# Performance work log

Hardware: AMD Instinct MI355X
Metric: run time of the kernel (lower is better)

The kernel has to match this reference:

```python
import jax, jax.numpy as jnp
import numpy as np

T, B, IN, OUT = 128, 32, 128, 128
N, M, R, H = 256, 64, 4, 256  # mem_slot, mem_size, read_heads, nn_output_size


def setup_inputs() -> dict:
    key = jax.random.key(0)
    ks = jax.random.split(key, 10)
    s = 0.05
    return {
        "xs": jax.random.normal(ks[0], (T, B, IN), jnp.float32),
        "mem0": jax.random.normal(ks[1], (B, N, M), jnp.float32) * s,
        "W_lstm": jax.random.normal(ks[2], (IN + M * R + H, 4 * H), jnp.float32) * s,
        "b_lstm": jnp.zeros((4 * H,), jnp.float32),
        "W_pre": jax.random.normal(ks[3], (H, OUT), jnp.float32) * s,
        "b_pre": jnp.zeros((OUT,), jnp.float32),
        "W_key": jax.random.normal(ks[4], (H, M), jnp.float32) * s,
        "W_beta": jax.random.normal(ks[5], (H, 1), jnp.float32) * s,
        "W_teach": jax.random.normal(ks[6], (H, M), jnp.float32) * s,
        "W_ro": jax.random.normal(ks[7], (M * R, OUT), jnp.float32) * s,
    }


def reference(xs, mem0, W_lstm, b_lstm, W_pre, b_pre, W_key, W_beta, W_teach, W_ro):
    eps = 1e-8

    def step(carry, x):
        mem, h, c, read_vecs, loss = carry
        # controller: LSTM cell over [x, flattened read vectors]
        inp = jnp.concatenate([x, read_vecs.reshape(B, M * R)], axis=-1)
        z = jnp.concatenate([inp, h], axis=-1) @ W_lstm + b_lstm
        i, f, g, o = jnp.split(z, 4, axis=-1)
        c = jax.nn.sigmoid(f) * c + jax.nn.sigmoid(i) * jnp.tanh(g)
        h = jax.nn.sigmoid(o) * jnp.tanh(c)
        pre_out = h @ W_pre + b_pre          # (B, OUT)
        k = h @ W_key                        # (B, M) content key
        beta = jax.nn.softplus(h @ W_beta)   # (B, 1) sharpness
        teacher = h @ W_teach                # (B, M) generated teacher vec
        # cosine similarity between each memory slot and the key
        num = jnp.einsum('bnm,bm->bn', mem, k)
        den = jnp.maximum(
            jnp.linalg.norm(mem, axis=-1) * jnp.linalg.norm(k, axis=-1, keepdims=True), eps)
        sim = num / den                      # (B, N)
        write_w = jax.nn.softmax(beta * sim, axis=-1)  # safe_softmax over slots
        # additive content write (outer product of write weights and key)
        mem = mem + write_w[:, :, None] * k[:, None, :]
        # supervision loss: match generated teacher to written content
        loss = loss + jnp.mean((k - teacher) ** 2)
        # read: write_w broadcast over R heads -> identical reads per head
        read = jnp.einsum('bn,bnm->bm', write_w, mem)  # (B, M)
        read_vecs = jnp.broadcast_to(read[:, :, None], (B, M, R))
        out = pre_out + read_vecs.reshape(B, M * R) @ W_ro
        return (mem, h, c, read_vecs, loss), out

    carry0 = (mem0,
              jnp.zeros((B, H), xs.dtype),
              jnp.zeros((B, H), xs.dtype),
              jnp.zeros((B, M, R), xs.dtype),
              jnp.zeros((), xs.dtype))
    (_, _, _, _, sup_loss), ys = jax.lax.scan(step, carry0, xs)
    return ys, sup_loss
```

## Files before the change

kernel.cpp:

```cpp
#include <hip/hip_runtime.h>

typedef unsigned short u16;
typedef unsigned long long u64;
typedef short short8 __attribute__((ext_vector_type(8)));
typedef float f32x4 __attribute__((ext_vector_type(4)));

__device__ __forceinline__ float b2f(u16 u) {
    unsigned x = ((unsigned)u) << 16;
    return __builtin_bit_cast(float, x);
}
__device__ __forceinline__ u16 f2b(float f) {
    unsigned u = __builtin_bit_cast(unsigned, f);
    u += 0x7FFFu + ((u >> 16) & 1u);
    return (u16)(u >> 16);
}
__device__ __forceinline__ float sigm(float x) { return 1.f / (1.f + __expf(-x)); }
__device__ __forceinline__ float tanh_(float x) { return 1.f - 2.f / (__expf(2.f * x) + 1.f); }

__device__ __forceinline__ uint4 ldg_cv(const void* p) {
    uint4 v;
    asm volatile("global_load_dwordx4 %0, %1, off sc0 sc1\n\ts_waitcnt vmcnt(0)"
                 : "=v"(v) : "v"(p) : "memory");
    return v;
}
__device__ __forceinline__ void ldg_cv4_issue(const void* p0, const void* p1, const void* p2,
                                              const void* p3, uint4& a, uint4& b, uint4& c, uint4& d) {
    asm volatile(
        "global_load_dwordx4 %0, %4, off sc0 sc1\n\t"
        "global_load_dwordx4 %1, %5, off sc0 sc1\n\t"
        "global_load_dwordx4 %2, %6, off sc0 sc1\n\t"
        "global_load_dwordx4 %3, %7, off sc0 sc1"
        : "=v"(a), "=v"(b), "=v"(c), "=v"(d)
        : "v"(p0), "v"(p1), "v"(p2), "v"(p3) : "memory");
}
__device__ __forceinline__ void wait_vm0() {
    asm volatile("s_waitcnt vmcnt(0)" ::: "memory");
}
__device__ __forceinline__ void stg_cv(void* p, uint4 v) {
    u64 lo = ((u64)v.y << 32) | (u64)v.x;
    u64 hi = ((u64)v.w << 32) | (u64)v.z;
    __hip_atomic_store((u64*)p,     lo, __ATOMIC_RELAXED, __HIP_MEMORY_SCOPE_AGENT);
    __hip_atomic_store((u64*)p + 1, hi, __ATOMIC_RELAXED, __HIP_MEMORY_SCOPE_AGENT);
}

#define T_STEPS 128
#define BATCH   32
#define KHR     320
#define PADK    328
#define MEMPAD  68
#define WKPAD   264

#define WS_BAR      0
#define WS_LOSS     128
#define WS_FLAG     160
#define WS_HRG      192
#define WS_ZSET     41088
#define WS_XSF      41216
#define WS_MEM0F    2138368
#define WS_WLF      4235520
#define WS_BLF      6856960
#define WS_WPREF    6861056
#define WS_BPREF    6992128
#define WS_WKEYF    6992640
#define WS_WBETAF   7058176
#define WS_WTEACHF  7059200
#define WS_WROF     7124736
#define WS_XW       7255808
#define WS_WREFF    24033024
#define WS_WKT      24295168
#define WS_WROEFF   24360704
#define WS_HS       24393472
#define WS_RS       28587776

#define HR_OFF   0
#define WF_OFF   20992
#define WK_OFF   41472
#define MEM_OFF  75264
#define Z_OFF    144896
#define C_OFF    149504
#define KV_OFF   151552
#define WW_OFF   151808
#define KP_OFF   152832
#define RP_OFF   153856
#define BR_OFF   154880
#define WR_OFF   154944
#define SC_OFF   155008
#define WB_OFF   155072
#define HST_OFF  156096
#define RST_OFF  156608
#define LDS_TOTAL 156736

__device__ __forceinline__ void gridbar(unsigned* flags, unsigned phase) {
    __syncthreads();
    if (threadIdx.x < 64) {
        if (threadIdx.x == 0)
            __hip_atomic_store(flags + blockIdx.x, phase, __ATOMIC_RELAXED,
                               __HIP_MEMORY_SCOPE_AGENT);
        long guard = 0;
        for (;;) {
            unsigned v = __hip_atomic_load(flags + (threadIdx.x & 31), __ATOMIC_RELAXED,
                                           __HIP_MEMORY_SCOPE_AGENT);
            if (__ballot(v < phase) == 0ull) break;
            if (++guard > 2000000L) break;
            __builtin_amdgcn_s_sleep(1);
        }
    }
    __syncthreads();
}

__global__ void dnc_probe(const u16* __restrict__ xs_u16, char* __restrict__ ws) {
    __shared__ int cnt;
    if (threadIdx.x == 0) cnt = 0;
    __syncthreads();
    int c = 0;
    for (int i = threadIdx.x; i < 1024; i += 256) {
        int e = (xs_u16[i] >> 7) & 0xFF;
        if (e >= 96 && e <= 135) c++;
    }
    atomicAdd(&cnt, c);
    __syncthreads();
    if (threadIdx.x == 0) *(int*)(ws + WS_FLAG) = (cnt > 820) ? 1 : 0;
}

__global__ void dnc_normalize(const void* s0, const void* s1, const void* s2, const void* s3,
                              const void* s4, const void* s5, const void* s6, const void* s7,
                              const void* s8, const void* s9, char* __restrict__ ws) {
    const void* srcs[10] = {s0, s1, s2, s3, s4, s5, s6, s7, s8, s9};
    const int sizes[10] = {524288, 524288, 655360, 1024, 32768, 128, 16384, 256, 16384, 32768};
    const int bases[10] = {WS_XSF, WS_MEM0F, WS_WLF, WS_BLF, WS_WPREF, WS_BPREF,
                           WS_WKEYF, WS_WBETAF, WS_WTEACHF, WS_WROF};
    const int bf = *(const int*)(ws + WS_FLAG);
    const int gt = blockIdx.x * 256 + threadIdx.x, gs = gridDim.x * 256;
    for (int s = 0; s < 10; ++s) {
        float* dst = (float*)(ws + bases[s]);
        const int n = sizes[s];
        if (bf) {
            const u16* p = (const u16*)srcs[s];
            for (int i = gt; i < n; i += gs) dst[i] = b2f(p[i]);
        } else {
            const float* p = (const float*)srcs[s];
            for (int i = gt; i < n; i += gs) dst[i] = p[i];
        }
    }
}

__global__ void dnc_prologue(char* __restrict__ ws) {
    extern __shared__ float xls[];
    const float* XSF     = (const float*)(ws + WS_XSF);
    const float* WLF     = (const float*)(ws + WS_WLF);
    const float* BLF     = (const float*)(ws + WS_BLF);
    const float* WKEYF   = (const float*)(ws + WS_WKEYF);
    const float* WTEACHF = (const float*)(ws + WS_WTEACHF);
    const float* WROF    = (const float*)(ws + WS_WROF);
    float* xW  = (float*)(ws + WS_XW);
    float* WrE = (float*)(ws + WS_WREFF);
    float* Wkt = (float*)(ws + WS_WKT);
    float* Wre = (float*)(ws + WS_WROEFF);
    const int wg = blockIdx.x, tid = threadIdx.x;
    if (wg < 256) {
        const int rb = wg >> 3, cb = wg & 7;
        const float4* xsrc = (const float4*)(XSF + (size_t)rb * 16384);
        for (int i = tid; i < 4096; i += 256) {
            float4 v = xsrc[i];
            int row = i >> 5, c4 = (i & 31) * 4;
            float* d = xls + row * 129 + c4;
            d[0] = v.x; d[1] = v.y; d[2] = v.z; d[3] = v.w;
        }
        __syncthreads();
        const int tr = tid >> 4, tc = tid & 15;
        const int c0 = cb * 128 + tc * 8;
        float acc[8][8];
#pragma unroll
        for (int rr = 0; rr < 8; ++rr)
#pragma unroll
            for (int cc = 0; cc < 8; ++cc) acc[rr][cc] = BLF[c0 + cc];
        for (int k = 0; k < 128; ++k) {
            float4 wA = *(const float4*)(WLF + (size_t)k * 1024 + c0);
            float4 wB = *(const float4*)(WLF + (size_t)k * 1024 + c0 + 4);
            float w[8] = {wA.x, wA.y, wA.z, wA.w, wB.x, wB.y, wB.z, wB.w};
#pragma unroll
            for (int rr = 0; rr < 8; ++rr) {
                float xv = xls[(tr * 8 + rr) * 129 + k];
#pragma unroll
                for (int cc = 0; cc < 8; ++cc) acc[rr][cc] += xv * w[cc];
            }
        }
#pragma unroll
        for (int rr = 0; rr < 8; ++rr) {
            size_t o = (size_t)(rb * 128 + tr * 8 + rr) * 1024 + c0;
            *(float4*)(xW + o)     = make_float4(acc[rr][0], acc[rr][1], acc[rr][2], acc[rr][3]);
            *(float4*)(xW + o + 4) = make_float4(acc[rr][4], acc[rr][5], acc[rr][6], acc[rr][7]);
        }
    } else if (wg < 320) {
        const int m = wg - 256;
        const int c = tid * 4;
#pragma unroll
        for (int e = 0; e < 4; ++e) {
            float s = 0.f;
#pragma unroll
            for (int rr = 0; rr < 4; ++rr) s += WLF[(size_t)(128 + 4 * m + rr) * 1024 + c + e];
            WrE[m * 1024 + c + e] = s;
        }
    } else if (wg < 336) {
        const int i = (wg - 320) * 1024 + tid * 4;
#pragma unroll
        for (int e = 0; e < 4; ++e) Wkt[i + e] = WKEYF[i + e] - WTEACHF[i + e];
    } else if (wg < 344) {
        const int i = (wg - 336) * 1024 + tid * 4;
#pragma unroll
        for (int e = 0; e < 4; ++e) {
            int m = (i + e) >> 7, c = (i + e) & 127;
            float s = 0.f;
#pragma unroll
            for (int rr = 0; rr < 4; ++rr) s += WROF[(4 * m + rr) * 128 + c];
            Wre[i + e] = s;
        }
    }
}

__global__ __launch_bounds__(256, 1) void dnc_main(char* __restrict__ ws) {
    extern __shared__ char smem[];
    u16*   hr_lds = (u16*)(smem + HR_OFF);
    u16*   wfrag  = (u16*)(smem + WF_OFF);
    u16*   wkeyT  = (u16*)(smem + WK_OFF);
    float* memA   = (float*)(smem + MEM_OFF);
    float* z_lds  = (float*)(smem + Z_OFF);
    float* c_lds  = (float*)(smem + C_OFF);
    float* kv     = (float*)(smem + KV_OFF);
    float* wwts   = (float*)(smem + WW_OFF);
    float* kpart  = (float*)(smem + KP_OFF);
    float* rp     = (float*)(smem + RP_OFF);
    float* bred   = (float*)(smem + BR_OFF);
    float* wred   = (float*)(smem + WR_OFF);
    float* sc     = (float*)(smem + SC_OFF);
    float* wbF    = (float*)(smem + WB_OFF);
    u16*   hstage = (u16*)(smem + HST_OFF);
    u16*   rstage = (u16*)(smem + RST_OFF);

    const int tid  = threadIdx.x;
    const int wg   = blockIdx.x;
    const int lane = tid & 63;
    const int wid  = tid >> 6;

    unsigned* flags = (unsigned*)(ws + WS_BAR);
    u16* hrg        = (u16*)(ws + WS_HRG);
    const float* xWF     = (const float*)(ws + WS_XW);
    const float* WrEffF  = (const float*)(ws + WS_WREFF);
    const float* WLF     = (const float*)(ws + WS_WLF);
    const float* WKEYF   = (const float*)(ws + WS_WKEYF);
    const float* WBETAF  = (const float*)(ws + WS_WBETAF);
    const float* MEM0F   = (const float*)(ws + WS_MEM0F);
    float* HsF = (float*)(ws + WS_HS);
    float* RsF = (float*)(ws + WS_RS);

    for (int i = tid; i < 32 * PADK; i += 256) hr_lds[i] = 0;
    for (int idx = tid; idx < 10240; idx += 256) {
        int k = idx >> 5, c = idx & 31;
        int kt = k >> 5, q = (k >> 3) & 3, j = k & 7;
        int gcol = (c >> 3) * 256 + wg * 8 + (c & 7);
        float v = (k < 64) ? WrEffF[k * 1024 + gcol]
                           : WLF[(size_t)(384 + (k - 64)) * 1024 + gcol];
        wfrag[((kt * 4 + q) * 32 + c) * 8 + j] = f2b(v);
    }
    for (int i = tid; i < 256 * 64; i += 256) {
        int k = i >> 6, m = i & 63;
        wkeyT[m * WKPAD + k] = f2b(WKEYF[i]);
    }
    wbF[tid]   = WBETAF[tid];
    c_lds[tid] = 0.f;
    for (int i = tid; i < 256 * 64; i += 256) {
        int n = i >> 6, m = i & 63;
        memA[n * MEMPAD + m] = MEM0F[wg * 16384 + i];
    }
    __syncthreads();

    const int bt = wid & 1, ct = wid >> 1;
    const int fm = lane & 15, fq = lane >> 4;
    const int pb = tid >> 3, pu = tid & 7;
    unsigned bar_phase = 0;

    float xg0, xg1, xg2, xg3;
    {
        const size_t xb = (size_t)pb * 1024 + wg * 8 + pu;
        xg0 = xWF[xb]; xg1 = xWF[xb + 256]; xg2 = xWF[xb + 512]; xg3 = xWF[xb + 768];
    }
    f32x4 hWacc = {0.f, 0.f, 0.f, 0.f};

    for (int t = 0; t < T_STEPS; ++t) {
        {
            uint4 rv = ldg_cv(hrg + pb * KHR + pu * 8);
            *(uint4*)(hr_lds + pb * PADK + pu * 8) = rv;
        }
        __syncthreads();

        f32x4 acc = hWacc;
#pragma unroll
        for (int kt = 0; kt < 2; ++kt) {
            short8 a = *(const short8*)(hr_lds + (bt * 16 + fm) * PADK + kt * 32 + fq * 8);
            short8 b = *(const short8*)(wfrag + ((kt * 4 + fq) * 32 + ct * 16 + fm) * 8);
            acc = __builtin_amdgcn_mfma_f32_16x16x32_bf16(a, b, acc, 0, 0, 0);
        }
#pragma unroll
        for (int r = 0; r < 4; ++r) {
            int bb = bt * 16 + fq * 4 + r;
            int cc = ct * 16 + fm;
            z_lds[bb * 36 + cc] = acc[r];
        }
        __syncthreads();

        {
            float iv = z_lds[pb * 36 + pu]      + xg0;
            float fv = z_lds[pb * 36 + 8 + pu]  + xg1;
            float gv = z_lds[pb * 36 + 16 + pu] + xg2;
            float ov = z_lds[pb * 36 + 24 + pu] + xg3;
            float co = c_lds[pb * 8 + pu];
            float cn = sigm(fv) * co + sigm(iv) * tanh_(gv);
            float hn = sigm(ov) * tanh_(cn);
            c_lds[pb * 8 + pu] = cn;
            hstage[pb * 8 + pu] = f2b(hn);
            HsF[(size_t)(t * BATCH + pb) * 256 + wg * 8 + pu] = hn;
        }
        __syncthreads();
        if (tid < 32) {
            uint4 hv = *(const uint4*)(hstage + tid * 8);
            stg_cv(hrg + tid * KHR + 64 + wg * 8, hv);
        }
        gridbar(flags, ++bar_phase);

        uint4 ha, hb4, hc, hd;
        {
            const u16* src = hrg + pb * KHR + 64 + pu * 32;
            ldg_cv4_issue(src, src + 8, src + 16, src + 24, ha, hb4, hc, hd);
        }
        {
            int tn = (t + 1 < T_STEPS) ? t + 1 : 127;
            const size_t xb = (size_t)(tn * BATCH + pb) * 1024 + wg * 8 + pu;
            xg0 = xWF[xb]; xg1 = xWF[xb + 256]; xg2 = xWF[xb + 512]; xg3 = xWF[xb + 768];
        }
        float nr2 = 0.f;
        {
            const float4* mrow = (const float4*)(memA + tid * MEMPAD);
#pragma unroll
            for (int i = 0; i < 16; ++i) {
                float4 m4 = mrow[i];
                nr2 += m4.x * m4.x + m4.y * m4.y + m4.z * m4.z + m4.w * m4.w;
            }
        }
        wait_vm0();
        {
            u16* dst = hr_lds + pb * PADK + 64 + pu * 32;
            *(uint4*)(dst)      = ha;
            *(uint4*)(dst + 8)  = hb4;
            *(uint4*)(dst + 16) = hc;
            *(uint4*)(dst + 24) = hd;
        }
        __syncthreads();

        {
            f32x4 hz = {0.f, 0.f, 0.f, 0.f};
#pragma unroll
            for (int kt = 2; kt < 10; ++kt) {
                short8 a = *(const short8*)(hr_lds + (bt * 16 + fm) * PADK + kt * 32 + fq * 8);
                short8 b = *(const short8*)(wfrag + ((kt * 4 + fq) * 32 + ct * 16 + fm) * 8);
                hz = __builtin_amdgcn_mfma_f32_16x16x32_bf16(a, b, hz, 0, 0, 0);
            }
            hWacc = hz;
        }

        const u16* hrow = hr_lds + wg * PADK + 64;
        {
            float a = 0.f;
#pragma unroll
            for (int i = 0; i < 8; ++i) {
                short8 w8 = *(const short8*)(wkeyT + lane * WKPAD + wid * 64 + i * 8);
                short8 h8 = *(const short8*)(hrow + wid * 64 + i * 8);
#pragma unroll
                for (int e = 0; e < 8; ++e)
                    a += b2f((u16)h8[e]) * b2f((u16)w8[e]);
            }
            kpart[wid * 64 + lane] = a;
        }
        {
            float bp = b2f(hrow[tid]) * wbF[tid];
#pragma unroll
            for (int off = 32; off > 0; off >>= 1) bp += __shfl_xor(bp, off, 64);
            if (lane == 0) bred[wid] = bp;
        }
        __syncthreads();
        if (tid < 64) {
            float kk = kpart[tid] + kpart[64 + tid] + kpart[128 + tid] + kpart[192 + tid];
            kv[tid] = kk;
            float k2 = kk * kk;
#pragma unroll
            for (int off = 32; off > 0; off >>= 1) k2 += __shfl_xor(k2, off, 64);
            if (tid == 0) sc[1] = sqrtf(k2);
        } else if (tid == 64) {
            float zb = bred[0] + bred[1] + bred[2] + bred[3];
            sc[0] = logf(1.f + __expf(zb));
        }
        __syncthreads();
        const float beta = sc[0], knorm = sc[1];

        float num = 0.f;
        {
            const float4* mrow = (const float4*)(memA + tid * MEMPAD);
            const float4* k4p  = (const float4*)kv;
#pragma unroll
            for (int i = 0; i < 16; ++i) {
                float4 m4 = mrow[i], k4 = k4p[i];
                num += m4.x * k4.x + m4.y * k4.y + m4.z * k4.z + m4.w * k4.w;
            }
        }
        float den = fmaxf(sqrtf(nr2) * knorm, 1e-8f);
        float s   = beta * (num / den);
        float wm = s;
#pragma unroll
        for (int off = 32; off > 0; off >>= 1) wm = fmaxf(wm, __shfl_xor(wm, off, 64));
        float ev = __expf(s - wm);
        float wsum = ev;
#pragma unroll
        for (int off = 32; off > 0; off >>= 1) wsum += __shfl_xor(wsum, off, 64);
        if (lane == 0) { wred[wid] = wm; wred[8 + wid] = wsum; }
        __syncthreads();
        float gm = fmaxf(fmaxf(wred[0], wred[1]), fmaxf(wred[2], wred[3]));
        float gsum = wred[8]  * __expf(wred[0] - gm) + wred[9]  * __expf(wred[1] - gm)
                   + wred[10] * __expf(wred[2] - gm) + wred[11] * __expf(wred[3] - gm);
        float w = __expf(s - gm) / gsum;
        wwts[tid] = w;
        __syncthreads();

        {
            const int lm = lane & 15, q = lane >> 4;
            float4 k4 = ((const float4*)kv)[lm];
            float r0 = 0.f, r1 = 0.f, r2 = 0.f, r3 = 0.f;
#pragma unroll
            for (int i = 0; i < 16; ++i) {
                int n = wid * 64 + i * 4 + q;
                float wn = wwts[n];
                float4* mp = (float4*)(memA + n * MEMPAD + 4 * lm);
                float4 m4 = *mp;
                m4.x += wn * k4.x; m4.y += wn * k4.y; m4.z += wn * k4.z; m4.w += wn * k4.w;
                *mp = m4;
                r0 += wn * m4.x; r1 += wn * m4.y; r2 += wn * m4.z; r3 += wn * m4.w;
            }
            r0 += __shfl_xor(r0, 16, 64); r0 += __shfl_xor(r0, 32, 64);
            r1 += __shfl_xor(r1, 16, 64); r1 += __shfl_xor(r1, 32, 64);
            r2 += __shfl_xor(r2, 16, 64); r2 += __shfl_xor(r2, 32, 64);
            r3 += __shfl_xor(r3, 16, 64); r3 += __shfl_xor(r3, 32, 64);
            if (q == 0) {
                rp[wid * 64 + 4 * lm + 0] = r0;
                rp[wid * 64 + 4 * lm + 1] = r1;
                rp[wid * 64 + 4 * lm + 2] = r2;
                rp[wid * 64 + 4 * lm + 3] = r3;
            }
        }
        __syncthreads();
        if (tid < 64) {
            float rd = rp[tid] + rp[64 + tid] + rp[128 + tid] + rp[192 + tid];
            rstage[tid] = f2b(rd);
            RsF[(size_t)(t * BATCH + wg) * 64 + tid] = rd;
        }
        __syncthreads();
        if (tid < 8) {
            uint4 rv = *(const uint4*)(rstage + tid * 8);
            stg_cv(hrg + wg * KHR + tid * 8, rv);
        }
        gridbar(flags, ++bar_phase);
    }
}

__global__ void dnc_epilogue(char* __restrict__ ws, void* __restrict__ outv) {
    __shared__ float hs8[8][256];
    __shared__ float rs8[8][64];
    __shared__ float lacc;
    const float* HsF   = (const float*)(ws + WS_HS);
    const float* RsF   = (const float*)(ws + WS_RS);
    const float* WktF  = (const float*)(ws + WS_WKT);
    const float* WreF  = (const float*)(ws + WS_WROEFF);
    const float* WpreF = (const float*)(ws + WS_WPREF);
    const float* bpreF = (const float*)(ws + WS_BPREF);
    float* lossacc = (float*)(ws + WS_LOSS);
    const int bf = *(const int*)(ws + WS_FLAG);
    const int tid = threadIdx.x;
    const size_t r0 = (size_t)blockIdx.x * 8;
    if (tid == 0) lacc = 0.f;
    for (int i = tid; i < 8 * 256; i += 256) hs8[i >> 8][i & 255] = HsF[r0 * 256 + i];
    for (int i = tid; i < 8 * 64; i += 256)  rs8[i >> 6][i & 63]  = RsF[r0 * 64 + i];
    __syncthreads();
    {
        const int rl = tid >> 5, c0 = (tid & 31) * 4;
        float a0 = bpreF[c0], a1 = bpreF[c0 + 1], a2 = bpreF[c0 + 2], a3 = bpreF[c0 + 3];
        for (int k = 0; k < 256; ++k) {
            float hv = hs8[rl][k];
            float4 w4 = *(const float4*)(WpreF + k * 128 + c0);
            a0 += hv * w4.x; a1 += hv * w4.y; a2 += hv * w4.z; a3 += hv * w4.w;
        }
        for (int m = 0; m < 64; ++m) {
            float rv = rs8[rl][m];
            float4 w4 = *(const float4*)(WreF + m * 128 + c0);
            a0 += rv * w4.x; a1 += rv * w4.y; a2 += rv * w4.z; a3 += rv * w4.w;
        }
        size_t o = (r0 + rl) * 128 + c0;
        if (bf) {
            u16* out = (u16*)outv;
            out[o] = f2b(a0); out[o + 1] = f2b(a1); out[o + 2] = f2b(a2); out[o + 3] = f2b(a3);
        } else {
            float* out = (float*)outv;
            out[o] = a0; out[o + 1] = a1; out[o + 2] = a2; out[o + 3] = a3;
        }
    }
    {
        const int rl = tid >> 5, m0 = (tid & 31) * 2;
        float d0 = 0.f, d1 = 0.f;
        for (int k = 0; k < 256; ++k) {
            float hv = hs8[rl][k];
            d0 += hv * WktF[k * 64 + m0];
            d1 += hv * WktF[k * 64 + m0 + 1];
        }
        float p = d0 * d0 + d1 * d1;
#pragma unroll
        for (int off = 32; off > 0; off >>= 1) p += __shfl_xor(p, off, 64);
        if ((tid & 63) == 0) atomicAdd(&lacc, p);
        __syncthreads();
        if (tid == 0) atomicAdd(lossacc, lacc);
    }
}

__global__ void dnc_loss_fin(const char* __restrict__ ws, void* __restrict__ outv) {
    if (threadIdx.x == 0 && blockIdx.x == 0) {
        float l = *(const float*)(ws + WS_LOSS) * (1.f / 2048.f);
        if (*(const int*)(ws + WS_FLAG)) ((u16*)outv)[524288] = f2b(l);
        else                             ((float*)outv)[524288] = l;
    }
}

extern "C" void kernel_launch(void* const* d_in, const int* in_sizes, int n_in,
                              void* d_out, int out_size, void* d_ws, size_t ws_size,
                              hipStream_t stream) {
    char* ws = (char*)d_ws;
    hipMemsetAsync(d_ws, 0, WS_ZSET, stream);
    dnc_probe<<<1, 256, 0, stream>>>((const u16*)d_in[0], ws);
    dnc_normalize<<<512, 256, 0, stream>>>(d_in[0], d_in[1], d_in[2], d_in[3], d_in[4],
                                           d_in[5], d_in[6], d_in[7], d_in[8], d_in[9], ws);
    (void)hipFuncSetAttribute((const void*)dnc_prologue,
                              hipFuncAttributeMaxDynamicSharedMemorySize, 128 * 129 * 4);
    dnc_prologue<<<344, 256, 128 * 129 * 4, stream>>>(ws);
    (void)hipFuncSetAttribute((const void*)dnc_main,
                              hipFuncAttributeMaxDynamicSharedMemorySize, LDS_TOTAL);
    dnc_main<<<32, 256, LDS_TOTAL, stream>>>(ws);
    dnc_epilogue<<<512, 256, 0, stream>>>(ws, d_out);
    dnc_loss_fin<<<1, 64, 0, stream>>>(ws, d_out);
}
```

Measured before the change: 1.163 ms.

## Replace grid barriers with tagged double-buffered data exchange

Removes both per-step grid-wide flag barriers. Each workgroup instead publishes its h and read-vector chunks as 64-bit words that carry a step tag, in double-buffered global slots. Consumers spin directly on the data words until the expected tag appears, so each block waits only for the data it needs rather than for every block. This adds more atomic polling traffic and wider payload words. It relies on 64-bit atomic stores being seen as single units, and the spin loops have guards that can give up silently.

After: 1.301 ms. 1.12x slower.

```diff
diff --git a/kernel.cpp b/kernel.cpp
--- a/kernel.cpp
+++ b/kernel.cpp
@@ -1,6 +1,7 @@
 #include <hip/hip_runtime.h>
 
 typedef unsigned short u16;
+typedef unsigned int u32;
 typedef unsigned long long u64;
 typedef short short8 __attribute__((ext_vector_type(8)));
 typedef float f32x4 __attribute__((ext_vector_type(4)));
@@ -17,30 +18,11 @@
 __device__ __forceinline__ float sigm(float x) { return 1.f / (1.f + __expf(-x)); }
 __device__ __forceinline__ float tanh_(float x) { return 1.f - 2.f / (__expf(2.f * x) + 1.f); }
 
-__device__ __forceinline__ uint4 ldg_cv(const void* p) {
-    uint4 v;
-    asm volatile("global_load_dwordx4 %0, %1, off sc0 sc1\n\ts_waitcnt vmcnt(0)"
-                 : "=v"(v) : "v"(p) : "memory");
-    return v;
-}
-__device__ __forceinline__ void ldg_cv4_issue(const void* p0, const void* p1, const void* p2,
-                                              const void* p3, uint4& a, uint4& b, uint4& c, uint4& d) {
-    asm volatile(
-        "global_load_dwordx4 %0, %4, off sc0 sc1\n\t"
-        "global_load_dwordx4 %1, %5, off sc0 sc1\n\t"
-        "global_load_dwordx4 %2, %6, off sc0 sc1\n\t"
-        "global_load_dwordx4 %3, %7, off sc0 sc1"
-        : "=v"(a), "=v"(b), "=v"(c), "=v"(d)
-        : "v"(p0), "v"(p1), "v"(p2), "v"(p3) : "memory");
-}
-__device__ __forceinline__ void wait_vm0() {
-    asm volatile("s_waitcnt vmcnt(0)" ::: "memory");
-}
-__device__ __forceinline__ void stg_cv(void* p, uint4 v) {
-    u64 lo = ((u64)v.y << 32) | (u64)v.x;
-    u64 hi = ((u64)v.w << 32) | (u64)v.z;
-    __hip_atomic_store((u64*)p,     lo, __ATOMIC_RELAXED, __HIP_MEMORY_SCOPE_AGENT);
-    __hip_atomic_store((u64*)p + 1, hi, __ATOMIC_RELAXED, __HIP_MEMORY_SCOPE_AGENT);
+__device__ __forceinline__ u64 lda(const u64* p) {
+    return __hip_atomic_load(p, __ATOMIC_RELAXED, __HIP_MEMORY_SCOPE_AGENT);
+}
+__device__ __forceinline__ void sta(u64* p, u64 v) {
+    __hip_atomic_store(p, v, __ATOMIC_RELAXED, __HIP_MEMORY_SCOPE_AGENT);
 }
 
 #define T_STEPS 128
@@ -50,27 +32,27 @@
 #define MEMPAD  68
 #define WKPAD   264
 
-#define WS_BAR      0
 #define WS_LOSS     128
 #define WS_FLAG     160
-#define WS_HRG      192
-#define WS_ZSET     41088
-#define WS_XSF      41216
-#define WS_MEM0F    2138368
-#define WS_WLF      4235520
-#define WS_BLF      6856960
-#define WS_WPREF    6861056
-#define WS_BPREF    6992128
-#define WS_WKEYF    6992640
-#define WS_WBETAF   7058176
-#define WS_WTEACHF  7059200
-#define WS_WROF     7124736
-#define WS_XW       7255808
-#define WS_WREFF    24033024
-#define WS_WKT      24295168
-#define WS_WROEFF   24360704
-#define WS_HS       24393472
-#define WS_RS       28587776
+#define WS_HT       1280
+#define WS_RT       66816
+#define WS_ZSET     83200
+#define WS_XSF      83968
+#define WS_MEM0F    2181120
+#define WS_WLF      4278272
+#define WS_BLF      6899712
+#define WS_WPREF    6903808
+#define WS_BPREF    7034880
+#define WS_WKEYF    7035392
+#define WS_WBETAF   7100928
+#define WS_WTEACHF  7101952
+#define WS_WROF     7167488
+#define WS_XW       7298560
+#define WS_WREFF    24075776
+#define WS_WKT      24337920
+#define WS_WROEFF   24403456
+#define WS_HS       24436224
+#define WS_RS       28630528
 
 #define HR_OFF   0
 #define WF_OFF   20992
@@ -89,24 +71,6 @@
 #define HST_OFF  156096
 #define RST_OFF  156608
 #define LDS_TOTAL 156736
-
-__device__ __forceinline__ void gridbar(unsigned* flags, unsigned phase) {
-    __syncthreads();
-    if (threadIdx.x < 64) {
-        if (threadIdx.x == 0)
-            __hip_atomic_store(flags + blockIdx.x, phase, __ATOMIC_RELAXED,
-                               __HIP_MEMORY_SCOPE_AGENT);
-        long guard = 0;
-        for (;;) {
-            unsigned v = __hip_atomic_load(flags + (threadIdx.x & 31), __ATOMIC_RELAXED,
-                                           __HIP_MEMORY_SCOPE_AGENT);
-            if (__ballot(v < phase) == 0ull) break;
-            if (++guard > 2000000L) break;
-            __builtin_amdgcn_s_sleep(1);
-        }
-    }
-    __syncthreads();
-}
 
 __global__ void dnc_probe(const u16* __restrict__ xs_u16, char* __restrict__ ws) {
     __shared__ int cnt;
@@ -242,8 +206,8 @@
     const int lane = tid & 63;
     const int wid  = tid >> 6;
 
-    unsigned* flags = (unsigned*)(ws + WS_BAR);
-    u16* hrg        = (u16*)(ws + WS_HRG);
+    u64* hT = (u64*)(ws + WS_HT);
+    u64* rT = (u64*)(ws + WS_RT);
     const float* xWF     = (const float*)(ws + WS_XW);
     const float* WrEffF  = (const float*)(ws + WS_WREFF);
     const float* WLF     = (const float*)(ws + WS_WLF);
@@ -277,7 +241,6 @@
     const int bt = wid & 1, ct = wid >> 1;
     const int fm = lane & 15, fq = lane >> 4;
     const int pb = tid >> 3, pu = tid & 7;
-    unsigned bar_phase = 0;
 
     float xg0, xg1, xg2, xg3;
     {
@@ -288,8 +251,20 @@
 
     for (int t = 0; t < T_STEPS; ++t) {
         {
-            uint4 rv = ldg_cv(hrg + pb * KHR + pu * 8);
-            *(uint4*)(hr_lds + pb * PADK + pu * 8) = rv;
+            const u64* rch = rT + (size_t)((((t + 1) & 1) * 32 + pb) * 16 + 2 * pu) * 2;
+            const u32 want = (u32)t;
+            u64 v0, v1, v2, v3;
+            long guard = 0;
+            for (;;) {
+                v0 = lda(rch); v1 = lda(rch + 1); v2 = lda(rch + 2); v3 = lda(rch + 3);
+                bool ok = ((u32)v0 == want) && ((u32)(v1 >> 32) == want) &&
+                          ((u32)v2 == want) && ((u32)(v3 >> 32) == want);
+                if (ok) break;
+                if (++guard > 100000L) break;
+            }
+            u32* dst = (u32*)hr_lds + pb * 164 + 4 * pu;
+            dst[0] = (u32)(v0 >> 32); dst[1] = (u32)v1;
+            dst[2] = (u32)(v2 >> 32); dst[3] = (u32)v3;
         }
         __syncthreads();
 
@@ -321,40 +296,54 @@
             HsF[(size_t)(t * BATCH + pb) * 256 + wg * 8 + pu] = hn;
         }
         __syncthreads();
-        if (tid < 32) {
-            uint4 hv = *(const uint4*)(hstage + tid * 8);
-            stg_cv(hrg + tid * KHR + 64 + wg * 8, hv);
-        }
-        gridbar(flags, ++bar_phase);
-
-        uint4 ha, hb4, hc, hd;
-        {
-            const u16* src = hrg + pb * KHR + 64 + pu * 32;
-            ldg_cv4_issue(src, src + 8, src + 16, src + 24, ha, hb4, hc, hd);
-        }
+        if (tid < 64) {
+            const int b = tid >> 1, c = tid & 1;
+            const u32* hs32 = (const u32*)hstage;
+            u32 w0 = hs32[b * 4 + 2 * c], w1 = hs32[b * 4 + 2 * c + 1];
+            u64* dstc = hT + (size_t)((((t & 1) * 32 + b) * 32 + wg) * 2 + c) * 2;
+            const u64 tag = (u64)(u32)(t + 1);
+            sta(dstc,     ((u64)w0 << 32) | tag);
+            sta(dstc + 1, (tag << 32) | w1);
+        }
+
+        float nr2 = 0.f;
+        {
+            const float4* mrow = (const float4*)(memA + tid * MEMPAD);
+#pragma unroll
+            for (int i = 0; i < 16; ++i) {
+                float4 m4 = mrow[i];
+                nr2 += m4.x * m4.x + m4.y * m4.y + m4.z * m4.z + m4.w * m4.w;
+            }
+        }
+        {
+            const u64* hch = hT + (size_t)((((t & 1) * 32 + pb) * 32 + 4 * pu) * 2) * 2;
+            const u32 want = (u32)(t + 1);
+            u64 v[16];
+            long guard = 0;
+            for (;;) {
+#pragma unroll
+                for (int i = 0; i < 16; ++i) v[i] = lda(hch + i);
+                bool ok = true;
+#pragma unroll
+                for (int i = 0; i < 8; ++i)
+                    ok = ok && ((u32)v[2 * i] == want) && ((u32)(v[2 * i + 1] >> 32) == want);
+                if (ok) break;
+                if (++guard > 100000L) break;
+            }
+            u32* dst = (u32*)hr_lds + pb * 164 + 32 + 16 * pu;
+#pragma unroll
+            for (int i = 0; i < 8; ++i) {
+                dst[2 * i]     = (u32)(v[2 * i] >> 32);
+                dst[2 * i + 1] = (u32)v[2 * i + 1];
+            }
+        }
+        __syncthreads();
+
         {
             int tn = (t + 1 < T_STEPS) ? t + 1 : 127;
             const size_t xb = (size_t)(tn * BATCH + pb) * 1024 + wg * 8 + pu;
             xg0 = xWF[xb]; xg1 = xWF[xb + 256]; xg2 = xWF[xb + 512]; xg3 = xWF[xb + 768];
         }
-        float nr2 = 0.f;
-        {
-            const float4* mrow = (const float4*)(memA + tid * MEMPAD);
-#pragma unroll
-            for (int i = 0; i < 16; ++i) {
-                float4 m4 = mrow[i];
-                nr2 += m4.x * m4.x + m4.y * m4.y + m4.z * m4.z + m4.w * m4.w;
-            }
-        }
-        wait_vm0();
-        {
-            u16* dst = hr_lds + pb * PADK + 64 + pu * 32;
-            *(uint4*)(dst)      = ha;
-            *(uint4*)(dst + 8)  = hb4;
-            *(uint4*)(dst + 16) = hc;
-            *(uint4*)(dst + 24) = hd;
-        }
-        __syncthreads();
 
         {
             f32x4 hz = {0.f, 0.f, 0.f, 0.f};
@@ -461,11 +450,14 @@
             RsF[(size_t)(t * BATCH + wg) * 64 + tid] = rd;
         }
         __syncthreads();
-        if (tid < 8) {
-            uint4 rv = *(const uint4*)(rstage + tid * 8);
-            stg_cv(hrg + wg * KHR + tid * 8, rv);
-        }
-        gridbar(flags, ++bar_phase);
+        if (tid < 16) {
+            const u32* rs32 = (const u32*)rstage;
+            u32 w0 = rs32[2 * tid], w1 = rs32[2 * tid + 1];
+            u64* dstc = rT + (size_t)(((t & 1) * 32 + wg) * 16 + tid) * 2;
+            const u64 tag = (u64)(u32)(t + 1);
+            sta(dstc,     ((u64)w0 << 32) | tag);
+            sta(dstc + 1, (tag << 32) | w1);
+        }
     }
 }
 
```

## Replace second grid barrier with tagged read-vector mailbox and defer memory update

Applied to the files above, without the earlier changes.

Drops the second per-step grid barrier. Each block now publishes its read vector into a double-buffered mailbox where every 32-bit payload sits next to a step tag, and consumers spin until the tags match instead of waiting for all blocks. The read is rewritten algebraically as w·mem_old + (Σw²)k, so the memory update can happen after the read vector is published, taking it off the critical path. The sleep is also removed from the barrier spin. The cost is more polling traffic and twice the global bytes for the read vectors, plus a changed floating-point summation order.

Result: faster. 1.076 ms (-7.5%).

```diff
diff --git a/kernel.cpp b/kernel.cpp
--- a/kernel.cpp
+++ b/kernel.cpp
@@ -1,6 +1,7 @@
 #include <hip/hip_runtime.h>
 
 typedef unsigned short u16;
+typedef unsigned int u32;
 typedef unsigned long long u64;
 typedef short short8 __attribute__((ext_vector_type(8)));
 typedef float f32x4 __attribute__((ext_vector_type(4)));
@@ -17,14 +18,20 @@
 __device__ __forceinline__ float sigm(float x) { return 1.f / (1.f + __expf(-x)); }
 __device__ __forceinline__ float tanh_(float x) { return 1.f - 2.f / (__expf(2.f * x) + 1.f); }
 
-__device__ __forceinline__ uint4 ldg_cv(const void* p) {
-    uint4 v;
-    asm volatile("global_load_dwordx4 %0, %1, off sc0 sc1\n\ts_waitcnt vmcnt(0)"
-                 : "=v"(v) : "v"(p) : "memory");
-    return v;
-}
-__device__ __forceinline__ void ldg_cv4_issue(const void* p0, const void* p1, const void* p2,
-                                              const void* p3, uint4& a, uint4& b, uint4& c, uint4& d) {
+__device__ __forceinline__ u64 lda(const u64* p) {
+    return __hip_atomic_load(p, __ATOMIC_RELAXED, __HIP_MEMORY_SCOPE_AGENT);
+}
+__device__ __forceinline__ void sta(u64* p, u64 v) {
+    __hip_atomic_store(p, v, __ATOMIC_RELAXED, __HIP_MEMORY_SCOPE_AGENT);
+}
+__device__ __forceinline__ unsigned ld_flag(const unsigned* p) {
+    return __hip_atomic_load(p, __ATOMIC_RELAXED, __HIP_MEMORY_SCOPE_AGENT);
+}
+__device__ __forceinline__ void st_flag(unsigned* p, unsigned v) {
+    __hip_atomic_store(p, v, __ATOMIC_RELAXED, __HIP_MEMORY_SCOPE_AGENT);
+}
+__device__ __forceinline__ void ld16x4_issue(const void* p0, const void* p1, const void* p2,
+                                             const void* p3, uint4& a, uint4& b, uint4& c, uint4& d) {
     asm volatile(
         "global_load_dwordx4 %0, %4, off sc0 sc1\n\t"
         "global_load_dwordx4 %1, %5, off sc0 sc1\n\t"
@@ -36,7 +43,7 @@
 __device__ __forceinline__ void wait_vm0() {
     asm volatile("s_waitcnt vmcnt(0)" ::: "memory");
 }
-__device__ __forceinline__ void stg_cv(void* p, uint4 v) {
+__device__ __forceinline__ void st16(void* p, uint4 v) {
     u64 lo = ((u64)v.y << 32) | (u64)v.x;
     u64 hi = ((u64)v.w << 32) | (u64)v.z;
     __hip_atomic_store((u64*)p,     lo, __ATOMIC_RELAXED, __HIP_MEMORY_SCOPE_AGENT);
@@ -53,7 +60,8 @@
 #define WS_BAR      0
 #define WS_LOSS     128
 #define WS_FLAG     160
-#define WS_HRG      192
+#define WS_RT       192
+#define WS_HRG      16576
 #define WS_ZSET     41088
 #define WS_XSF      41216
 #define WS_MEM0F    2138368
@@ -90,19 +98,15 @@
 #define RST_OFF  156608
 #define LDS_TOTAL 156736
 
-__device__ __forceinline__ void gridbar(unsigned* flags, unsigned phase) {
+__device__ __forceinline__ void gridbar(unsigned* flags, unsigned phase, int rank) {
     __syncthreads();
     if (threadIdx.x < 64) {
-        if (threadIdx.x == 0)
-            __hip_atomic_store(flags + blockIdx.x, phase, __ATOMIC_RELAXED,
-                               __HIP_MEMORY_SCOPE_AGENT);
+        if (threadIdx.x == 0) st_flag(flags + rank, phase);
         long guard = 0;
         for (;;) {
-            unsigned v = __hip_atomic_load(flags + (threadIdx.x & 31), __ATOMIC_RELAXED,
-                                           __HIP_MEMORY_SCOPE_AGENT);
+            unsigned v = ld_flag(flags + (threadIdx.x & 31));
             if (__ballot(v < phase) == 0ull) break;
-            if (++guard > 2000000L) break;
-            __builtin_amdgcn_s_sleep(1);
+            if (++guard > 1000000L) break;
         }
     }
     __syncthreads();
@@ -243,6 +247,7 @@
     const int wid  = tid >> 6;
 
     unsigned* flags = (unsigned*)(ws + WS_BAR);
+    u64* rT         = (u64*)(ws + WS_RT);
     u16* hrg        = (u16*)(ws + WS_HRG);
     const float* xWF     = (const float*)(ws + WS_XW);
     const float* WrEffF  = (const float*)(ws + WS_WREFF);
@@ -277,7 +282,6 @@
     const int bt = wid & 1, ct = wid >> 1;
     const int fm = lane & 15, fq = lane >> 4;
     const int pb = tid >> 3, pu = tid & 7;
-    unsigned bar_phase = 0;
 
     float xg0, xg1, xg2, xg3;
     {
@@ -288,8 +292,20 @@
 
     for (int t = 0; t < T_STEPS; ++t) {
         {
-            uint4 rv = ldg_cv(hrg + pb * KHR + pu * 8);
-            *(uint4*)(hr_lds + pb * PADK + pu * 8) = rv;
+            const u64* rch = rT + (size_t)((((t + 1) & 1) * 32 + pb) * 16 + 2 * pu) * 2;
+            const u32 want = (u32)t;
+            u64 v0, v1, v2, v3;
+            long guard = 0;
+            for (;;) {
+                v0 = lda(rch); v1 = lda(rch + 1); v2 = lda(rch + 2); v3 = lda(rch + 3);
+                bool ok = ((u32)v0 == want) && ((u32)(v1 >> 32) == want) &&
+                          ((u32)v2 == want) && ((u32)(v3 >> 32) == want);
+                if (ok) break;
+                if (++guard > 200000L) break;
+            }
+            u32* dst = (u32*)hr_lds + pb * 164 + 4 * pu;
+            dst[0] = (u32)(v0 >> 32); dst[1] = (u32)v1;
+            dst[2] = (u32)(v2 >> 32); dst[3] = (u32)v3;
         }
         __syncthreads();
 
@@ -323,14 +339,14 @@
         __syncthreads();
         if (tid < 32) {
             uint4 hv = *(const uint4*)(hstage + tid * 8);
-            stg_cv(hrg + tid * KHR + 64 + wg * 8, hv);
-        }
-        gridbar(flags, ++bar_phase);
+            st16(hrg + tid * KHR + 64 + wg * 8, hv);
+        }
+        gridbar(flags, (unsigned)(t + 1), wg);
 
         uint4 ha, hb4, hc, hd;
         {
             const u16* src = hrg + pb * KHR + 64 + pu * 32;
-            ldg_cv4_issue(src, src + 8, src + 16, src + 24, ha, hb4, hc, hd);
+            ld16x4_issue(src, src + 8, src + 16, src + 24, ha, hb4, hc, hd);
         }
         {
             int tn = (t + 1 < T_STEPS) ? t + 1 : 127;
@@ -427,20 +443,23 @@
                    + wred[10] * __expf(wred[2] - gm) + wred[11] * __expf(wred[3] - gm);
         float w = __expf(s - gm) / gsum;
         wwts[tid] = w;
-        __syncthreads();
+        {
+            float w2 = w * w;
+#pragma unroll
+            for (int off = 32; off > 0; off >>= 1) w2 += __shfl_xor(w2, off, 64);
+            if (lane == 0) bred[wid] = w2;
+        }
+        __syncthreads();
+        const float wsq = bred[0] + bred[1] + bred[2] + bred[3];
 
         {
             const int lm = lane & 15, q = lane >> 4;
-            float4 k4 = ((const float4*)kv)[lm];
             float r0 = 0.f, r1 = 0.f, r2 = 0.f, r3 = 0.f;
 #pragma unroll
             for (int i = 0; i < 16; ++i) {
                 int n = wid * 64 + i * 4 + q;
                 float wn = wwts[n];
-                float4* mp = (float4*)(memA + n * MEMPAD + 4 * lm);
-                float4 m4 = *mp;
-                m4.x += wn * k4.x; m4.y += wn * k4.y; m4.z += wn * k4.z; m4.w += wn * k4.w;
-                *mp = m4;
+                float4 m4 = *(const float4*)(memA + n * MEMPAD + 4 * lm);
                 r0 += wn * m4.x; r1 += wn * m4.y; r2 += wn * m4.z; r3 += wn * m4.w;
             }
             r0 += __shfl_xor(r0, 16, 64); r0 += __shfl_xor(r0, 32, 64);
@@ -456,16 +475,33 @@
         }
         __syncthreads();
         if (tid < 64) {
-            float rd = rp[tid] + rp[64 + tid] + rp[128 + tid] + rp[192 + tid];
+            float rd = rp[tid] + rp[64 + tid] + rp[128 + tid] + rp[192 + tid]
+                     + wsq * kv[tid];
             rstage[tid] = f2b(rd);
             RsF[(size_t)(t * BATCH + wg) * 64 + tid] = rd;
         }
         __syncthreads();
-        if (tid < 8) {
-            uint4 rv = *(const uint4*)(rstage + tid * 8);
-            stg_cv(hrg + wg * KHR + tid * 8, rv);
-        }
-        gridbar(flags, ++bar_phase);
+        if (tid < 16) {
+            const u32* rs32 = (const u32*)rstage;
+            u32 w0 = rs32[2 * tid], w1 = rs32[2 * tid + 1];
+            u64* dstc = rT + (size_t)(((t & 1) * 32 + wg) * 16 + tid) * 2;
+            const u64 tag = (u64)(u32)(t + 1);
+            sta(dstc,     ((u64)w0 << 32) | tag);
+            sta(dstc + 1, (tag << 32) | w1);
+        }
+        {
+            const int lm = lane & 15, q = lane >> 4;
+            float4 k4 = ((const float4*)kv)[lm];
+#pragma unroll
+            for (int i = 0; i < 16; ++i) {
+                int n = wid * 64 + i * 4 + q;
+                float wn = wwts[n];
+                float4* mp = (float4*)(memA + n * MEMPAD + 4 * lm);
+                float4 m4 = *mp;
+                m4.x += wn * k4.x; m4.y += wn * k4.y; m4.z += wn * k4.z; m4.w += wn * k4.w;
+                *mp = m4;
+            }
+        }
     }
 }
 
```
